# Performance work log

Hardware: AMD Instinct MI355X
Metric: run time of the kernel (lower is better)

The kernel has to match this reference:

```python
import jax, jax.numpy as jnp
import numpy as np


def _conv3x3(x, W, b):
    # NCHW conv, stride 1, padding 1 (hard-coded in the torch module)
    y = jax.lax.conv_general_dilated(
        x, W, window_strides=(1, 1), padding=[(1, 1), (1, 1)],
        dimension_numbers=("NCHW", "OIHW", "NCHW"))
    return y + b[None, :, None, None]


def _grid_sample_bilinear(img, gx, gy):
    # img: [N,H,W]; gx,gy: [N,H,W] normalized coords in [-1,1].
    # Matches torch grid_sample(mode='bilinear', padding_mode='zeros',
    # align_corners=False).
    N, H, W = img.shape
    ix = ((gx + 1.0) * W - 1.0) * 0.5  # unnormalized x coord
    iy = ((gy + 1.0) * H - 1.0) * 0.5  # unnormalized y coord

    x0f = jnp.floor(ix)
    y0f = jnp.floor(iy)
    x0 = x0f.astype(jnp.int32)
    y0 = y0f.astype(jnp.int32)
    x1 = x0 + 1
    y1 = y0 + 1

    # bilinear weights
    wx1 = ix - x0f
    wy1 = iy - y0f
    wx0 = 1.0 - wx1
    wy0 = 1.0 - wy1

    n_idx = jnp.arange(N)[:, None, None]

    def gather(yi, xi):
        valid = (yi >= 0) & (yi < H) & (xi >= 0) & (xi < W)
        yc = jnp.clip(yi, 0, H - 1)
        xc = jnp.clip(xi, 0, W - 1)
        v = img[n_idx, yc, xc]
        return jnp.where(valid, v, 0.0)

    return (gather(y0, x0) * (wy0 * wx0)
            + gather(y0, x1) * (wy0 * wx1)
            + gather(y1, x0) * (wy1 * wx0)
            + gather(y1, x1) * (wy1 * wx1))


def setup_inputs() -> dict:
    key = jax.random.key(0)
    ks = jax.random.split(key, 7)
    B, Cin, Cout, H, W = 16, 64, 64, 128, 128
    fan_in = Cin * 3 * 3
    std = 1.0 / np.sqrt(fan_in)
    x = jax.random.normal(ks[0], (B, Cin, H, W), dtype=jnp.float32)
    Ws = jax.random.normal(ks[1], (Cout, Cin, 3, 3), dtype=jnp.float32) * std
    Wx = jax.random.normal(ks[2], (Cout, Cin, 3, 3), dtype=jnp.float32) * std
    Wy = jax.random.normal(ks[3], (Cout, Cin, 3, 3), dtype=jnp.float32) * std
    bs = jnp.zeros((Cout,), dtype=jnp.float32)
    bx = jnp.zeros((Cout,), dtype=jnp.float32)
    by = jnp.zeros((Cout,), dtype=jnp.float32)
    return {"x": x, "Ws": Ws, "bs": bs, "Wx": Wx, "bx": bx, "Wy": Wy, "by": by}


def reference(x, Ws, bs, Wx, bx, Wy, by):
    score = _conv3x3(x, Ws, bs)            # [B,C,H,W]
    gx = _conv3x3(x, Wx, bx)               # absolute grid x coords
    gy = _conv3x3(x, Wy, by)               # absolute grid y coords
    B, C, H, W = score.shape
    out = _grid_sample_bilinear(score.reshape(B * C, H, W),
                                gx.reshape(B * C, H, W),
                                gy.reshape(B * C, H, W))
    return out.reshape(B, C, H, W)
```

## Files before the change

### kernel.cpp

```cpp
#include <hip/hip_runtime.h>
#include <stdint.h>

typedef unsigned short ushort_t;
typedef _Float16 f16x8 __attribute__((ext_vector_type(8)));
typedef float f32x4 __attribute__((ext_vector_type(4)));
typedef float f32x16 __attribute__((ext_vector_type(16)));
typedef int   i32x4 __attribute__((ext_vector_type(4)));
typedef int   i32x16 __attribute__((ext_vector_type(16)));
typedef unsigned int uint4v __attribute__((ext_vector_type(4)));

#define HW_ 16384
#define MFMAH  __builtin_amdgcn_mfma_f32_32x32x16_f16
#define MFMAI8 __builtin_amdgcn_mfma_i32_32x32x32_i8
#define C_CORR (1.0f/16777216.0f)

__device__ __forceinline__ ushort_t f2h_bits(float f){
  union { _Float16 h; ushort_t u; } c; c.h = (_Float16)f; return c.u;
}
__device__ __forceinline__ float h_bits2f(ushort_t u){
  union { _Float16 h; ushort_t u; } c; c.u = u; return (float)c.h;
}
__device__ __forceinline__ int clamp8(int v){ return min(max(v,-127),127); }

__global__ __launch_bounds__(256) void k_repack(
    const float* __restrict__ Ws, const float* __restrict__ Wx,
    const float* __restrict__ Wy,
    ushort_t* __restrict__ WpH, unsigned int* __restrict__ WpC){
  int e = blockIdx.x*256 + threadIdx.x;
  if (e < 110592){
    int j = e & 7; int lane = (e >> 3) & 63; int rest = e >> 9;
    int ks = rest % 36; int cm = rest / 36;
    int conv = cm >> 1; int mh = cm & 1;
    int co = mh*32 + (lane & 31);
    int tap = ks >> 2;
    int ci = (ks & 3)*16 + ((lane >> 5) & 1)*8 + j;
    const float* src = (conv==0) ? Ws : (conv==1) ? Wx : Wy;
    WpH[e] = f2h_bits(src[(co*64 + ci)*9 + tap]);
  } else if (e < 110592 + 36864){
    int d = e - 110592;
    int j4 = d & 3; int lane = (d >> 2) & 63; int rest = d >> 8;
    int ks = rest % 18; int gm = rest / 18;
    int g = gm >> 1; int mh = gm & 1;
    int co = mh*32 + (lane & 31);
    int tap = ks >> 1;
    const float* src = (g==0 || g==2) ? Wx : Wy;
    unsigned dd = 0;
    #pragma unroll
    for (int bb=0; bb<4; bb++){
      int ci = (ks & 1)*32 + ((lane >> 5) & 1)*16 + j4*4 + bb;
      float w = src[(co*64 + ci)*9 + tap];
      int v;
      if (g < 2){
        v = clamp8((int)rintf(w*512.f));
      } else {
        float wl = w - h_bits2f(f2h_bits(w));
        v = clamp8((int)rintf(wl*1048576.f));
      }
      dd |= ((unsigned)(v & 255)) << (bb*8);
    }
    WpC[d] = dd;
  }
}

__global__ __launch_bounds__(256, 2) void k_conv_all(
    const float* __restrict__ x,
    const ushort_t* __restrict__ WpH, const unsigned int* __restrict__ WpC,
    const float* __restrict__ bs, const float* __restrict__ bx,
    const float* __restrict__ by,
    ushort_t* __restrict__ score, unsigned int* __restrict__ coords){
  int bid = blockIdx.x;
  int idx = bid >> 3;
  int b = (bid & 7) + 8*(idx >> 8);
  int rest = idx & 255;
  int h0 = (rest >> 2)*2;
  int wq = (rest & 3)*32;
  int t = threadIdx.x; int lane = t & 63; int wid = t >> 6;
  int n = lane & 31; int kh = lane >> 5;
  __shared__ __align__(16) _Float16 BH[4*34*64];
  __shared__ __align__(16) char BAl[4*34*64];
  __shared__ __align__(16) char BAh[4*34*64];

  const float* xb = x + (size_t)b*64*HW_;
  #pragma unroll
  for (int it=0; it<3; it++){
    int f = it*256 + t;
    if (f < 544){
      int r = f/136; int rem = f - r*136; int q = rem/34; int w1 = rem - q*34;
      int y = h0 + r - 1; int w = wq + w1 - 1;
      f16x8 h0v = {0,0,0,0,0,0,0,0}, h1v = {0,0,0,0,0,0,0,0};
      unsigned alb[4] = {0,0,0,0}, ahb[4] = {0,0,0,0};
      if (((unsigned)y < 128u) & ((unsigned)w < 128u)){
        const float* p = xb + (size_t)(q*16)*HW_ + y*128 + w;
        #pragma unroll
        for (int j=0; j<16; j++){
          float v = p[(size_t)j*HW_];
          _Float16 hv = (_Float16)v;
          float al = v - (float)hv;
          int a8 = clamp8((int)rintf(al*32768.f));
          int x8 = clamp8((int)rintf(v*16.f));
          if (j < 8) h0v[j] = hv; else h1v[j-8] = hv;
          alb[j>>2] |= ((unsigned)(a8 & 255)) << ((j&3)*8);
          ahb[j>>2] |= ((unsigned)(x8 & 255)) << ((j&3)*8);
        }
      }
      int base = (r*34 + w1)*64;
      int sw = w1 & 7;
      *(f16x8*)&BH[base + (((2*q)   ^ sw) << 3)] = h0v;
      *(f16x8*)&BH[base + (((2*q+1) ^ sw) << 3)] = h1v;
      int islot = ((q + (w1 >> 1)) & 3) << 4;
      i32x4 av  = {(int)alb[0],(int)alb[1],(int)alb[2],(int)alb[3]};
      i32x4 hv2 = {(int)ahb[0],(int)ahb[1],(int)ahb[2],(int)ahb[3]};
      *(i32x4*)&BAl[base + islot] = av;
      *(i32x4*)&BAh[base + islot] = hv2;
    }
  }
  __syncthreads();

  int mh = wid & 1;
  int ph = wid >> 1;

  f32x16 acc_s, acc_gx, acc_gy;
  i32x16 c_x, c_y;
  #pragma unroll
  for (int r2=0; r2<16; r2++){
    acc_s[r2]=0.f; acc_gx[r2]=0.f; acc_gy[r2]=0.f; c_x[r2]=0; c_y[r2]=0;
  }

  const ushort_t* aS = WpH + ((0*2+mh)*36)*512 + lane*8;
  const ushort_t* aX = WpH + ((1*2+mh)*36)*512 + lane*8;
  const ushort_t* aY = WpH + ((2*2+mh)*36)*512 + lane*8;
  const char* cWhx = (const char*)WpC + (((0*2+mh)*18)*64 + lane)*16;
  const char* cWhy = (const char*)WpC + (((1*2+mh)*18)*64 + lane)*16;
  const char* cWlx = (const char*)WpC + (((2*2+mh)*18)*64 + lane)*16;
  const char* cWly = (const char*)WpC + (((3*2+mh)*18)*64 + lane)*16;

  #pragma unroll
  for (int tap=0; tap<9; tap++){
    int rb = tap/3; int dw = tap - rb*3 - 1;
    int row = rb + ph;
    int w1 = n + dw + 1;
    int rowb = (row*34 + w1)*64;
    int sw = w1 & 7;
    int islotbase = (w1 >> 1);
    #pragma unroll
    for (int qp=0; qp<2; qp++){
      int ksA  = tap*4 + qp*2;
      int ks32 = tap*2 + qp;
      f16x8 sA = *(const f16x8*)&aS[ksA*512];
      f16x8 sB = *(const f16x8*)&aS[(ksA+1)*512];
      f16x8 xA = *(const f16x8*)&aX[ksA*512];
      f16x8 xB = *(const f16x8*)&aX[(ksA+1)*512];
      f16x8 yA = *(const f16x8*)&aY[ksA*512];
      f16x8 yB = *(const f16x8*)&aY[(ksA+1)*512];
      i32x4 whx = *(const i32x4*)&cWhx[ks32*1024];
      i32x4 why = *(const i32x4*)&cWhy[ks32*1024];
      i32x4 wlx = *(const i32x4*)&cWlx[ks32*1024];
      i32x4 wly = *(const i32x4*)&cWly[ks32*1024];
      f16x8 bA = *(const f16x8*)&BH[rowb + (((qp*4 + kh)     ^ sw) << 3)];
      f16x8 bB = *(const f16x8*)&BH[rowb + (((qp*4 + 2 + kh) ^ sw) << 3)];
      int islot = (((qp*2 + kh) + islotbase) & 3) << 4;
      i32x4 bal = *(const i32x4*)&BAl[rowb + islot];
      i32x4 bah = *(const i32x4*)&BAh[rowb + islot];
      acc_s  = MFMAH(sA, bA, acc_s,  0,0,0);
      acc_gx = MFMAH(xA, bA, acc_gx, 0,0,0);
      acc_gy = MFMAH(yA, bA, acc_gy, 0,0,0);
      acc_s  = MFMAH(sB, bB, acc_s,  0,0,0);
      acc_gx = MFMAH(xB, bB, acc_gx, 0,0,0);
      acc_gy = MFMAH(yB, bB, acc_gy, 0,0,0);
      c_x = MFMAI8(whx, bal, c_x, 0,0,0);
      c_x = MFMAI8(wlx, bah, c_x, 0,0,0);
      c_y = MFMAI8(why, bal, c_y, 0,0,0);
      c_y = MFMAI8(wly, bah, c_y, 0,0,0);
    }
  }

  int h = h0 + ph;
  int w = wq + n;
  ushort_t*     sb = score  + (size_t)b*64*HW_ + h*128 + w;
  unsigned int* cb = coords + (size_t)b*64*HW_ + h*128 + w;
  #pragma unroll
  for (int reg=0; reg<16; reg++){
    int col = mh*32 + (reg & 3) + 8*(reg >> 2) + 4*kh;
    float sv = acc_s[reg] + bs[col];
    float gx = acc_gx[reg] + (float)c_x[reg]*C_CORR + bx[col];
    float gy = acc_gy[reg] + (float)c_y[reg]*C_CORR + by[col];
    sb[(size_t)col*HW_] = f2h_bits(sv);
    float ix = fminf(fmaxf((gx + 1.f)*64.f - 0.5f, -2.f), 129.f);
    float iy = fminf(fmaxf((gy + 1.f)*64.f - 0.5f, -2.f), 129.f);
    unsigned ux = (unsigned)rintf((ix + 2.f)*480.f);
    unsigned uy = (unsigned)rintf((iy + 2.f)*480.f);
    cb[(size_t)col*HW_] = ux | (uy << 16);
  }
}

__global__ __launch_bounds__(256, 4) void k_sample(
    const ushort_t* __restrict__ score, const unsigned int* __restrict__ coords,
    float* __restrict__ out){
  int bid = blockIdx.x;
  int idx = bid >> 3;
  int b  = (bid & 7) + 8*(idx >> 6);
  int co = idx & 63;
  int t = threadIdx.x;
  __shared__ __align__(16) ushort_t SC[128*136];

  const ushort_t* sp = score + (size_t)(b*64 + co)*HW_;
  #pragma unroll
  for (int i=0;i<8;i++){
    int c = i*256 + t;
    int y = c >> 4; int xg = (c & 15)*8;
    *(f16x8*)&SC[y*136 + xg] = *(const f16x8*)(sp + c*8);
  }
  __syncthreads();

  const unsigned int* cp = coords + (size_t)(b*64 + co)*HW_;
  float* op = out + (size_t)(b*64 + co)*HW_;
  uint4v ca = *(const uint4v*)(cp + t*8);
  uint4v cb2 = *(const uint4v*)(cp + t*8 + 4);
  #pragma unroll 1
  for (int k=0;k<8;k++){
    int px = (k*256 + t)*8;
    uint4v na, nb;
    if (k < 7){
      na = *(const uint4v*)(cp + px + 2048);
      nb = *(const uint4v*)(cp + px + 2052);
    }
    float r[8];
    #pragma unroll
    for (int j=0;j<8;j++){
      unsigned u = (j < 4) ? ca[j] : cb2[j-4];
      float ix = (float)(u & 0xffffu)*(1.0f/480.0f) - 2.0f;
      float iy = (float)(u >> 16)   *(1.0f/480.0f) - 2.0f;
      float x0f = floorf(ix), y0f = floorf(iy);
      int x0 = (int)x0f, y0 = (int)y0f;
      float wx1 = ix - x0f, wy1 = iy - y0f;
      float wx0 = 1.f - wx1, wy0 = 1.f - wy1;
      int x0c = min(max(x0,0),127), x1c = min(max(x0+1,0),127);
      int y0c = min(max(y0,0),127), y1c = min(max(y0+1,0),127);
      bool vx0 = (unsigned)x0     < 128u, vx1 = (unsigned)(x0+1) < 128u;
      bool vy0 = (unsigned)y0     < 128u, vy1 = (unsigned)(y0+1) < 128u;
      float v00 = (vy0 && vx0) ? h_bits2f(SC[y0c*136 + x0c]) : 0.f;
      float v01 = (vy0 && vx1) ? h_bits2f(SC[y0c*136 + x1c]) : 0.f;
      float v10 = (vy1 && vx0) ? h_bits2f(SC[y1c*136 + x0c]) : 0.f;
      float v11 = (vy1 && vx1) ? h_bits2f(SC[y1c*136 + x1c]) : 0.f;
      r[j] = v00*(wy0*wx0) + v01*(wy0*wx1) + v10*(wy1*wx0) + v11*(wy1*wx1);
    }
    f32x4 r0 = {r[0],r[1],r[2],r[3]};
    f32x4 r1 = {r[4],r[5],r[6],r[7]};
    *(f32x4*)(op + px)     = r0;
    *(f32x4*)(op + px + 4) = r1;
    ca = na; cb2 = nb;
  }
}

extern "C" void kernel_launch(void* const* d_in, const int* in_sizes, int n_in,
                              void* d_out, int out_size, void* d_ws, size_t ws_size,
                              hipStream_t stream){
  const float* x  = (const float*)d_in[0];
  const float* Ws = (const float*)d_in[1];
  const float* bs = (const float*)d_in[2];
  const float* Wx = (const float*)d_in[3];
  const float* bx = (const float*)d_in[4];
  const float* Wy = (const float*)d_in[5];
  const float* by = (const float*)d_in[6];
  float* out = (float*)d_out;
  ushort_t* ws  = (ushort_t*)d_ws;
  ushort_t*     score  = ws;
  unsigned int* coords = (unsigned int*)(ws + 16777216);
  ushort_t*     WpH    = ws + 50331648;
  unsigned int* WpC    = (unsigned int*)(ws + 50331648 + 110592);

  k_repack  <<<dim3(576),  256, 0, stream>>>(Ws, Wx, Wy, WpH, WpC);
  k_conv_all<<<dim3(4096), 256, 0, stream>>>(x, WpH, WpC, bs, bx, by, score, coords);
  k_sample  <<<dim3(1024), 256, 0, stream>>>(score, coords, out);
}
```

Baseline: 292.5 us.

## Compute two output rows per wave in conv kernel to reuse weight fragments

Each conv block now covers four output rows instead of two, and each wave accumulates two rows at once. The weight A-fragments loaded from global memory are reused across both rows, halving weight traffic per output, and the halo overhead in the shared-memory input tile drops from 4 rows per 2 outputs to 6 per 4. The cost is doubled accumulator registers (ten 16-wide vectors), which may exceed the register budget for 2 blocks per CU, plus larger LDS tiles and half as many blocks.

```diff
diff --git a/kernel.cpp b/kernel.cpp
--- a/kernel.cpp
+++ b/kernel.cpp
@@ -70,21 +70,21 @@
     ushort_t* __restrict__ score, unsigned int* __restrict__ coords){
   int bid = blockIdx.x;
   int idx = bid >> 3;
-  int b = (bid & 7) + 8*(idx >> 8);
-  int rest = idx & 255;
-  int h0 = (rest >> 2)*2;
+  int b = (bid & 7) + 8*(idx >> 7);
+  int rest = idx & 127;
+  int h0 = (rest >> 2)*4;
   int wq = (rest & 3)*32;
   int t = threadIdx.x; int lane = t & 63; int wid = t >> 6;
   int n = lane & 31; int kh = lane >> 5;
-  __shared__ __align__(16) _Float16 BH[4*34*64];
-  __shared__ __align__(16) char BAl[4*34*64];
-  __shared__ __align__(16) char BAh[4*34*64];
+  __shared__ __align__(16) _Float16 BH[6*34*64];
+  __shared__ __align__(16) char BAl[6*34*64];
+  __shared__ __align__(16) char BAh[6*34*64];
 
   const float* xb = x + (size_t)b*64*HW_;
   #pragma unroll
-  for (int it=0; it<3; it++){
+  for (int it=0; it<4; it++){
     int f = it*256 + t;
-    if (f < 544){
+    if (f < 816){
       int r = f/136; int rem = f - r*136; int q = rem/34; int w1 = rem - q*34;
       int y = h0 + r - 1; int w = wq + w1 - 1;
       f16x8 h0v = {0,0,0,0,0,0,0,0}, h1v = {0,0,0,0,0,0,0,0};
@@ -117,13 +117,15 @@
   __syncthreads();
 
   int mh = wid & 1;
-  int ph = wid >> 1;
-
-  f32x16 acc_s, acc_gx, acc_gy;
-  i32x16 c_x, c_y;
+  int pp = wid >> 1;
+
+  f32x16 acc_s0, acc_gx0, acc_gy0, acc_s1, acc_gx1, acc_gy1;
+  i32x16 c_x0, c_y0, c_x1, c_y1;
   #pragma unroll
   for (int r2=0; r2<16; r2++){
-    acc_s[r2]=0.f; acc_gx[r2]=0.f; acc_gy[r2]=0.f; c_x[r2]=0; c_y[r2]=0;
+    acc_s0[r2]=0.f; acc_gx0[r2]=0.f; acc_gy0[r2]=0.f;
+    acc_s1[r2]=0.f; acc_gx1[r2]=0.f; acc_gy1[r2]=0.f;
+    c_x0[r2]=0; c_y0[r2]=0; c_x1[r2]=0; c_y1[r2]=0;
   }
 
   const ushort_t* aS = WpH + ((0*2+mh)*36)*512 + lane*8;
@@ -134,14 +136,31 @@
   const char* cWlx = (const char*)WpC + (((2*2+mh)*18)*64 + lane)*16;
   const char* cWly = (const char*)WpC + (((3*2+mh)*18)*64 + lane)*16;
 
+  #define ROWBLK(ROWB, AS_, AX_, AY_, CX_, CY_) do {                    \
+    f16x8 bA  = *(const f16x8*)&BH[(ROWB) + off0];                      \
+    f16x8 bB  = *(const f16x8*)&BH[(ROWB) + off1];                      \
+    i32x4 bal = *(const i32x4*)&BAl[(ROWB) + islot];                    \
+    i32x4 bah = *(const i32x4*)&BAh[(ROWB) + islot];                    \
+    AS_ = MFMAH(sA, bA, AS_, 0,0,0);                                    \
+    AX_ = MFMAH(xA, bA, AX_, 0,0,0);                                    \
+    AY_ = MFMAH(yA, bA, AY_, 0,0,0);                                    \
+    AS_ = MFMAH(sB, bB, AS_, 0,0,0);                                    \
+    AX_ = MFMAH(xB, bB, AX_, 0,0,0);                                    \
+    AY_ = MFMAH(yB, bB, AY_, 0,0,0);                                    \
+    CX_ = MFMAI8(whx, bal, CX_, 0,0,0);                                 \
+    CX_ = MFMAI8(wlx, bah, CX_, 0,0,0);                                 \
+    CY_ = MFMAI8(why, bal, CY_, 0,0,0);                                 \
+    CY_ = MFMAI8(wly, bah, CY_, 0,0,0);                                 \
+  } while(0)
+
   #pragma unroll
   for (int tap=0; tap<9; tap++){
     int rb = tap/3; int dw = tap - rb*3 - 1;
-    int row = rb + ph;
     int w1 = n + dw + 1;
-    int rowb = (row*34 + w1)*64;
     int sw = w1 & 7;
     int islotbase = (w1 >> 1);
+    int rowb0 = ((rb + 2*pp)*34 + w1)*64;
+    int rowb1 = rowb0 + 34*64;
     #pragma unroll
     for (int qp=0; qp<2; qp++){
       int ksA  = tap*4 + qp*2;
@@ -156,41 +175,37 @@
       i32x4 why = *(const i32x4*)&cWhy[ks32*1024];
       i32x4 wlx = *(const i32x4*)&cWlx[ks32*1024];
       i32x4 wly = *(const i32x4*)&cWly[ks32*1024];
-      f16x8 bA = *(const f16x8*)&BH[rowb + (((qp*4 + kh)     ^ sw) << 3)];
-      f16x8 bB = *(const f16x8*)&BH[rowb + (((qp*4 + 2 + kh) ^ sw) << 3)];
+      int off0  = ((qp*4 + kh)     ^ sw) << 3;
+      int off1  = ((qp*4 + 2 + kh) ^ sw) << 3;
       int islot = (((qp*2 + kh) + islotbase) & 3) << 4;
-      i32x4 bal = *(const i32x4*)&BAl[rowb + islot];
-      i32x4 bah = *(const i32x4*)&BAh[rowb + islot];
-      acc_s  = MFMAH(sA, bA, acc_s,  0,0,0);
-      acc_gx = MFMAH(xA, bA, acc_gx, 0,0,0);
-      acc_gy = MFMAH(yA, bA, acc_gy, 0,0,0);
-      acc_s  = MFMAH(sB, bB, acc_s,  0,0,0);
-      acc_gx = MFMAH(xB, bB, acc_gx, 0,0,0);
-      acc_gy = MFMAH(yB, bB, acc_gy, 0,0,0);
-      c_x = MFMAI8(whx, bal, c_x, 0,0,0);
-      c_x = MFMAI8(wlx, bah, c_x, 0,0,0);
-      c_y = MFMAI8(why, bal, c_y, 0,0,0);
-      c_y = MFMAI8(wly, bah, c_y, 0,0,0);
-    }
-  }
-
-  int h = h0 + ph;
+      ROWBLK(rowb0, acc_s0, acc_gx0, acc_gy0, c_x0, c_y0);
+      ROWBLK(rowb1, acc_s1, acc_gx1, acc_gy1, c_x1, c_y1);
+    }
+  }
+  #undef ROWBLK
+
   int w = wq + n;
-  ushort_t*     sb = score  + (size_t)b*64*HW_ + h*128 + w;
-  unsigned int* cb = coords + (size_t)b*64*HW_ + h*128 + w;
-  #pragma unroll
-  for (int reg=0; reg<16; reg++){
-    int col = mh*32 + (reg & 3) + 8*(reg >> 2) + 4*kh;
-    float sv = acc_s[reg] + bs[col];
-    float gx = acc_gx[reg] + (float)c_x[reg]*C_CORR + bx[col];
-    float gy = acc_gy[reg] + (float)c_y[reg]*C_CORR + by[col];
-    sb[(size_t)col*HW_] = f2h_bits(sv);
-    float ix = fminf(fmaxf((gx + 1.f)*64.f - 0.5f, -2.f), 129.f);
-    float iy = fminf(fmaxf((gy + 1.f)*64.f - 0.5f, -2.f), 129.f);
-    unsigned ux = (unsigned)rintf((ix + 2.f)*480.f);
-    unsigned uy = (unsigned)rintf((iy + 2.f)*480.f);
-    cb[(size_t)col*HW_] = ux | (uy << 16);
-  }
+  int hb = h0 + 2*pp;
+  #define EPILOG(AS_, AX_, AY_, CX_, CY_, H_) do {                      \
+    ushort_t*     sb = score  + (size_t)b*64*HW_ + (H_)*128 + w;        \
+    unsigned int* cb = coords + (size_t)b*64*HW_ + (H_)*128 + w;        \
+    _Pragma("unroll")                                                   \
+    for (int reg=0; reg<16; reg++){                                     \
+      int col = mh*32 + (reg & 3) + 8*(reg >> 2) + 4*kh;                \
+      float sv = AS_[reg] + bs[col];                                    \
+      float gx = AX_[reg] + (float)CX_[reg]*C_CORR + bx[col];           \
+      float gy = AY_[reg] + (float)CY_[reg]*C_CORR + by[col];           \
+      sb[(size_t)col*HW_] = f2h_bits(sv);                               \
+      float ixf = fminf(fmaxf((gx + 1.f)*64.f - 0.5f, -2.f), 129.f);    \
+      float iyf = fminf(fmaxf((gy + 1.f)*64.f - 0.5f, -2.f), 129.f);    \
+      unsigned ux = (unsigned)rintf((ixf + 2.f)*480.f);                 \
+      unsigned uy = (unsigned)rintf((iyf + 2.f)*480.f);                 \
+      cb[(size_t)col*HW_] = ux | (uy << 16);                            \
+    }                                                                   \
+  } while(0)
+  EPILOG(acc_s0, acc_gx0, acc_gy0, c_x0, c_y0, hb);
+  EPILOG(acc_s1, acc_gx1, acc_gy1, c_x1, c_y1, hb+1);
+  #undef EPILOG
 }
 
 __global__ __launch_bounds__(256, 4) void k_sample(
@@ -270,6 +285,6 @@
   unsigned int* WpC    = (unsigned int*)(ws + 50331648 + 110592);
 
   k_repack  <<<dim3(576),  256, 0, stream>>>(Ws, Wx, Wy, WpH, WpC);
-  k_conv_all<<<dim3(4096), 256, 0, stream>>>(x, WpH, WpC, bs, bx, by, score, coords);
+  k_conv_all<<<dim3(2048), 256, 0, stream>>>(x, WpH, WpC, bs, bx, by, score, coords);
   k_sample  <<<dim3(1024), 256, 0, stream>>>(score, coords, out);
 }
```

Measured after the change: 820.6 us. 2.81x slower.

## Split conv work across three wave groups, one per output convolution

Applied to the files above, without the earlier changes.

The conv kernel now launches 768 threads per block. Each group of four waves computes only one of the three convolutions (score, gx, or gy), where before every wave computed all three. Weight fragments are software-prefetched one k-step ahead, and the x/y coordinate halves are written as separate 16-bit stores. The aim is to cut per-thread register pressure and raise MFMA issue parallelism, at the cost of reading shared tiles three times and doing narrower global stores.

```diff
diff --git a/kernel.cpp b/kernel.cpp
--- a/kernel.cpp
+++ b/kernel.cpp
@@ -62,7 +62,7 @@
   }
 }
 
-__global__ __launch_bounds__(256, 2) void k_conv_all(
+__global__ __launch_bounds__(768, 3) void k_conv_all(
     const float* __restrict__ x,
     const ushort_t* __restrict__ WpH, const unsigned int* __restrict__ WpC,
     const float* __restrict__ bs, const float* __restrict__ bx,
@@ -81,115 +81,128 @@
   __shared__ __align__(16) char BAh[4*34*64];
 
   const float* xb = x + (size_t)b*64*HW_;
-  #pragma unroll
-  for (int it=0; it<3; it++){
-    int f = it*256 + t;
-    if (f < 544){
-      int r = f/136; int rem = f - r*136; int q = rem/34; int w1 = rem - q*34;
-      int y = h0 + r - 1; int w = wq + w1 - 1;
-      f16x8 h0v = {0,0,0,0,0,0,0,0}, h1v = {0,0,0,0,0,0,0,0};
-      unsigned alb[4] = {0,0,0,0}, ahb[4] = {0,0,0,0};
-      if (((unsigned)y < 128u) & ((unsigned)w < 128u)){
-        const float* p = xb + (size_t)(q*16)*HW_ + y*128 + w;
-        #pragma unroll
-        for (int j=0; j<16; j++){
-          float v = p[(size_t)j*HW_];
-          _Float16 hv = (_Float16)v;
-          float al = v - (float)hv;
-          int a8 = clamp8((int)rintf(al*32768.f));
-          int x8 = clamp8((int)rintf(v*16.f));
-          if (j < 8) h0v[j] = hv; else h1v[j-8] = hv;
-          alb[j>>2] |= ((unsigned)(a8 & 255)) << ((j&3)*8);
-          ahb[j>>2] |= ((unsigned)(x8 & 255)) << ((j&3)*8);
-        }
+  if (t < 544){
+    int f = t;
+    int r = f/136; int rem = f - r*136; int q = rem/34; int w1 = rem - q*34;
+    int y = h0 + r - 1; int w = wq + w1 - 1;
+    f16x8 h0v = {0,0,0,0,0,0,0,0}, h1v = {0,0,0,0,0,0,0,0};
+    unsigned alb[4] = {0,0,0,0}, ahb[4] = {0,0,0,0};
+    if (((unsigned)y < 128u) & ((unsigned)w < 128u)){
+      const float* p = xb + (size_t)(q*16)*HW_ + y*128 + w;
+      #pragma unroll
+      for (int j=0; j<16; j++){
+        float v = p[(size_t)j*HW_];
+        _Float16 hv = (_Float16)v;
+        float al = v - (float)hv;
+        int a8 = clamp8((int)rintf(al*32768.f));
+        int x8 = clamp8((int)rintf(v*16.f));
+        if (j < 8) h0v[j] = hv; else h1v[j-8] = hv;
+        alb[j>>2] |= ((unsigned)(a8 & 255)) << ((j&3)*8);
+        ahb[j>>2] |= ((unsigned)(x8 & 255)) << ((j&3)*8);
       }
-      int base = (r*34 + w1)*64;
-      int sw = w1 & 7;
-      *(f16x8*)&BH[base + (((2*q)   ^ sw) << 3)] = h0v;
-      *(f16x8*)&BH[base + (((2*q+1) ^ sw) << 3)] = h1v;
-      int islot = ((q + (w1 >> 1)) & 3) << 4;
-      i32x4 av  = {(int)alb[0],(int)alb[1],(int)alb[2],(int)alb[3]};
-      i32x4 hv2 = {(int)ahb[0],(int)ahb[1],(int)ahb[2],(int)ahb[3]};
-      *(i32x4*)&BAl[base + islot] = av;
-      *(i32x4*)&BAh[base + islot] = hv2;
-    }
+    }
+    int base = (r*34 + w1)*64;
+    int sw = w1 & 7;
+    *(f16x8*)&BH[base + (((2*q)   ^ sw) << 3)] = h0v;
+    *(f16x8*)&BH[base + (((2*q+1) ^ sw) << 3)] = h1v;
+    int islot = ((q + (w1 >> 1)) & 3) << 4;
+    i32x4 av  = {(int)alb[0],(int)alb[1],(int)alb[2],(int)alb[3]};
+    i32x4 hv2 = {(int)ahb[0],(int)ahb[1],(int)ahb[2],(int)ahb[3]};
+    *(i32x4*)&BAl[base + islot] = av;
+    *(i32x4*)&BAh[base + islot] = hv2;
   }
   __syncthreads();
 
-  int mh = wid & 1;
-  int ph = wid >> 1;
-
-  f32x16 acc_s, acc_gx, acc_gy;
-  i32x16 c_x, c_y;
-  #pragma unroll
-  for (int r2=0; r2<16; r2++){
-    acc_s[r2]=0.f; acc_gx[r2]=0.f; acc_gy[r2]=0.f; c_x[r2]=0; c_y[r2]=0;
-  }
-
-  const ushort_t* aS = WpH + ((0*2+mh)*36)*512 + lane*8;
-  const ushort_t* aX = WpH + ((1*2+mh)*36)*512 + lane*8;
-  const ushort_t* aY = WpH + ((2*2+mh)*36)*512 + lane*8;
-  const char* cWhx = (const char*)WpC + (((0*2+mh)*18)*64 + lane)*16;
-  const char* cWhy = (const char*)WpC + (((1*2+mh)*18)*64 + lane)*16;
-  const char* cWlx = (const char*)WpC + (((2*2+mh)*18)*64 + lane)*16;
-  const char* cWly = (const char*)WpC + (((3*2+mh)*18)*64 + lane)*16;
-
-  #pragma unroll
-  for (int tap=0; tap<9; tap++){
-    int rb = tap/3; int dw = tap - rb*3 - 1;
-    int row = rb + ph;
-    int w1 = n + dw + 1;
-    int rowb = (row*34 + w1)*64;
-    int sw = w1 & 7;
-    int islotbase = (w1 >> 1);
-    #pragma unroll
-    for (int qp=0; qp<2; qp++){
-      int ksA  = tap*4 + qp*2;
-      int ks32 = tap*2 + qp;
-      f16x8 sA = *(const f16x8*)&aS[ksA*512];
-      f16x8 sB = *(const f16x8*)&aS[(ksA+1)*512];
-      f16x8 xA = *(const f16x8*)&aX[ksA*512];
-      f16x8 xB = *(const f16x8*)&aX[(ksA+1)*512];
-      f16x8 yA = *(const f16x8*)&aY[ksA*512];
-      f16x8 yB = *(const f16x8*)&aY[(ksA+1)*512];
-      i32x4 whx = *(const i32x4*)&cWhx[ks32*1024];
-      i32x4 why = *(const i32x4*)&cWhy[ks32*1024];
-      i32x4 wlx = *(const i32x4*)&cWlx[ks32*1024];
-      i32x4 wly = *(const i32x4*)&cWly[ks32*1024];
-      f16x8 bA = *(const f16x8*)&BH[rowb + (((qp*4 + kh)     ^ sw) << 3)];
-      f16x8 bB = *(const f16x8*)&BH[rowb + (((qp*4 + 2 + kh) ^ sw) << 3)];
-      int islot = (((qp*2 + kh) + islotbase) & 3) << 4;
+  int conv   = wid >> 2;
+  int sub    = wid & 3;
+  int mh     = sub & 1;
+  int row_id = sub >> 1;
+
+  int w = wq + n;
+  int h = h0 + row_id;
+  size_t obase = (size_t)b*64*HW_ + (size_t)h*128 + w;
+
+  if (conv == 0){
+    f32x16 acc;
+    #pragma unroll
+    for (int r2=0; r2<16; r2++) acc[r2]=0.f;
+    const ushort_t* pF = WpH + ((0*2+mh)*36)*512 + lane*8;
+    f16x8 w0 = *(const f16x8*)pF;
+    f16x8 w1v = *(const f16x8*)(pF + 512);
+    #pragma unroll 2
+    for (int ks=0; ks<18; ++ks){
+      int tap = ks >> 1; int qp = ks & 1;
+      int rb = (tap*11) >> 5;
+      int dw = tap - rb*3 - 1;
+      int wc = n + dw + 1;
+      int sw = wc & 7;
+      int rowb = ((rb + row_id)*34 + wc)*64;
+      int off0 = ((qp*4 + kh)     ^ sw) << 3;
+      int off1 = ((qp*4 + 2 + kh) ^ sw) << 3;
+      f16x8 bA = *(const f16x8*)&BH[rowb + off0];
+      f16x8 bB = *(const f16x8*)&BH[rowb + off1];
+      int adv = (ks < 17) ? 1024 : 0;
+      f16x8 n0 = *(const f16x8*)(pF + adv);
+      f16x8 n1 = *(const f16x8*)(pF + adv + 512);
+      acc = MFMAH(w0,  bA, acc, 0,0,0);
+      acc = MFMAH(w1v, bB, acc, 0,0,0);
+      w0 = n0; w1v = n1; pF += adv;
+    }
+    #pragma unroll
+    for (int reg=0; reg<16; reg++){
+      int col = mh*32 + (reg & 3) + 8*(reg >> 2) + 4*kh;
+      float sv = acc[reg] + bs[col];
+      score[obase + (size_t)col*HW_] = f2h_bits(sv);
+    }
+  } else {
+    f32x16 acc; i32x16 c;
+    #pragma unroll
+    for (int r2=0; r2<16; r2++){ acc[r2]=0.f; c[r2]=0; }
+    const ushort_t* pF = WpH + ((conv*2+mh)*36)*512 + lane*8;
+    const char* pWh = (const char*)WpC + ((((conv-1)*2+mh)*18)*64 + lane)*16;
+    const char* pWl = (const char*)WpC + ((((conv+1)*2+mh)*18)*64 + lane)*16;
+    f16x8 w0 = *(const f16x8*)pF;
+    f16x8 w1v = *(const f16x8*)(pF + 512);
+    i32x4 wh = *(const i32x4*)pWh;
+    i32x4 wl = *(const i32x4*)pWl;
+    #pragma unroll 2
+    for (int ks=0; ks<18; ++ks){
+      int tap = ks >> 1; int qp = ks & 1;
+      int rb = (tap*11) >> 5;
+      int dw = tap - rb*3 - 1;
+      int wc = n + dw + 1;
+      int sw = wc & 7;
+      int rowb = ((rb + row_id)*34 + wc)*64;
+      int off0 = ((qp*4 + kh)     ^ sw) << 3;
+      int off1 = ((qp*4 + 2 + kh) ^ sw) << 3;
+      int islot = (((qp*2 + kh) + (wc >> 1)) & 3) << 4;
+      f16x8 bA  = *(const f16x8*)&BH[rowb + off0];
+      f16x8 bB  = *(const f16x8*)&BH[rowb + off1];
       i32x4 bal = *(const i32x4*)&BAl[rowb + islot];
       i32x4 bah = *(const i32x4*)&BAh[rowb + islot];
-      acc_s  = MFMAH(sA, bA, acc_s,  0,0,0);
-      acc_gx = MFMAH(xA, bA, acc_gx, 0,0,0);
-      acc_gy = MFMAH(yA, bA, acc_gy, 0,0,0);
-      acc_s  = MFMAH(sB, bB, acc_s,  0,0,0);
-      acc_gx = MFMAH(xB, bB, acc_gx, 0,0,0);
-      acc_gy = MFMAH(yB, bB, acc_gy, 0,0,0);
-      c_x = MFMAI8(whx, bal, c_x, 0,0,0);
-      c_x = MFMAI8(wlx, bah, c_x, 0,0,0);
-      c_y = MFMAI8(why, bal, c_y, 0,0,0);
-      c_y = MFMAI8(wly, bah, c_y, 0,0,0);
-    }
-  }
-
-  int h = h0 + ph;
-  int w = wq + n;
-  ushort_t*     sb = score  + (size_t)b*64*HW_ + h*128 + w;
-  unsigned int* cb = coords + (size_t)b*64*HW_ + h*128 + w;
-  #pragma unroll
-  for (int reg=0; reg<16; reg++){
-    int col = mh*32 + (reg & 3) + 8*(reg >> 2) + 4*kh;
-    float sv = acc_s[reg] + bs[col];
-    float gx = acc_gx[reg] + (float)c_x[reg]*C_CORR + bx[col];
-    float gy = acc_gy[reg] + (float)c_y[reg]*C_CORR + by[col];
-    sb[(size_t)col*HW_] = f2h_bits(sv);
-    float ix = fminf(fmaxf((gx + 1.f)*64.f - 0.5f, -2.f), 129.f);
-    float iy = fminf(fmaxf((gy + 1.f)*64.f - 0.5f, -2.f), 129.f);
-    unsigned ux = (unsigned)rintf((ix + 2.f)*480.f);
-    unsigned uy = (unsigned)rintf((iy + 2.f)*480.f);
-    cb[(size_t)col*HW_] = ux | (uy << 16);
+      int adv = (ks < 17) ? 1024 : 0;
+      f16x8 n0 = *(const f16x8*)(pF + adv);
+      f16x8 n1 = *(const f16x8*)(pF + adv + 512);
+      i32x4 nh = *(const i32x4*)(pWh + adv);
+      i32x4 nl = *(const i32x4*)(pWl + adv);
+      acc = MFMAH(w0,  bA, acc, 0,0,0);
+      acc = MFMAH(w1v, bB, acc, 0,0,0);
+      c = MFMAI8(wh, bal, c, 0,0,0);
+      c = MFMAI8(wl, bah, c, 0,0,0);
+      w0 = n0; w1v = n1; wh = nh; wl = nl;
+      pF += adv; pWh += adv; pWl += adv;
+    }
+    const float* bias = (conv == 1) ? bx : by;
+    int half = conv - 1;
+    #pragma unroll
+    for (int reg=0; reg<16; reg++){
+      int col = mh*32 + (reg & 3) + 8*(reg >> 2) + 4*kh;
+      float g = acc[reg] + (float)c[reg]*C_CORR + bias[col];
+      float iz = fminf(fmaxf((g + 1.f)*64.f - 0.5f, -2.f), 129.f);
+      unsigned uz = (unsigned)rintf((iz + 2.f)*480.f);
+      ushort_t* cw = (ushort_t*)(coords + obase + (size_t)col*HW_);
+      cw[half] = (ushort_t)uz;
+    }
   }
 }
 
@@ -270,6 +283,6 @@
   unsigned int* WpC    = (unsigned int*)(ws + 50331648 + 110592);
 
   k_repack  <<<dim3(576),  256, 0, stream>>>(Ws, Wx, Wy, WpH, WpC);
-  k_conv_all<<<dim3(4096), 256, 0, stream>>>(x, WpH, WpC, bs, bx, by, score, coords);
+  k_conv_all<<<dim3(4096), 768, 0, stream>>>(x, WpH, WpC, bs, bx, by, score, coords);
   k_sample  <<<dim3(1024), 256, 0, stream>>>(score, coords, out);
 }
```

After: 303.2 us. 1.04x slower.
